# Performance work log

Measured on AMD Instinct MI355X. Metric: run time of the kernel, lower is better.

The kernel has to match this reference:

```python
import jax, jax.numpy as jnp
import numpy as np

EPS = 1e-5

def gamma_layer_norm(x, gamma):
    # LayerNorm over last dim with learnable gamma only (no bias)
    mu = jnp.mean(x, axis=-1, keepdims=True)
    var = jnp.var(x, axis=-1, keepdims=True)
    return (x - mu) * jax.lax.rsqrt(var + EPS) * gamma

def setup_inputs() -> dict:
    key = jax.random.key(0)
    k1, k2, k3, k4 = jax.random.split(key, 4)
    b, n, dim = 8, 4096, 512
    heads, head_size = 8, 64
    hidden = heads * head_size  # 512
    x = jax.random.normal(k1, (b, n, dim), dtype=jnp.float32)
    # nn.Linear(dim, hidden*3, bias=False): weight [3*hidden, dim]
    w_qkv = jax.random.normal(k2, (3 * hidden, dim), dtype=jnp.float32) * (dim ** -0.5)
    # nn.Linear(hidden, dim, bias=False): weight [dim, hidden]
    w_out = jax.random.normal(k3, (dim, hidden), dtype=jnp.float32) * (hidden ** -0.5)
    gamma = 1.0 + 0.02 * jax.random.normal(k4, (dim,), dtype=jnp.float32)
    return {"x": x, "w_qkv": w_qkv, "w_out": w_out, "gamma": gamma}

def reference(x, w_qkv, w_out, gamma):
    b, n, dim = x.shape
    heads, head_size = 8, 64
    scale = head_size ** -0.5
    # norm=False -> Identity; no time conditioning
    qkv = jnp.einsum('bnd,hd->bnh', x, w_qkv)  # [b, n, 3*hidden]
    q, k, v = jnp.split(qkv, 3, axis=-1)
    def to_heads(t):
        return t.reshape(b, n, heads, head_size).transpose(0, 2, 1, 3)  # b h n d
    q, k, v = to_heads(q), to_heads(k), to_heads(v)
    q = jax.nn.softmax(q, axis=-1) * scale   # softmax over feature dim
    k = jax.nn.softmax(k, axis=-2)           # softmax over sequence dim
    context = jnp.einsum('bhnd,bhne->bhde', k, v)      # [b, h, d, e]
    out = jnp.einsum('bhde,bhnd->bhne', context, q)    # [b, h, n, e]
    out = out.transpose(0, 2, 1, 3).reshape(b, n, heads * head_size)
    out = jnp.einsum('bnh,dh->bnd', out, w_out)
    out = gamma_layer_norm(out, gamma)  # dropout inactive (p=0 / eval)
    return out
```

## Files before the change

kernel.cpp:

```cpp
#include <hip/hip_runtime.h>
#include <hip/hip_bf16.h>
#include <stdint.h>
#include <stddef.h>

typedef __bf16 bf16_t;
typedef __bf16 bf16x8 __attribute__((ext_vector_type(8)));
typedef float floatx4 __attribute__((ext_vector_type(4)));

#define DIM 512
#define SEQ 4096
#define BATCH 8

static __device__ __forceinline__ floatx4 mfma_bf16(bf16x8 a, bf16x8 b, floatx4 c) {
  return __builtin_amdgcn_mfma_f32_16x16x32_bf16(a, b, c, 0, 0, 0);
}

typedef __attribute__((address_space(1))) const void* gas_ptr;
typedef __attribute__((address_space(3))) void* las_ptr;
static __device__ __forceinline__ void gll16(const void* g, void* l) {
  __builtin_amdgcn_global_load_lds((gas_ptr)g, (las_ptr)l, 16, 0, 0);
}

__global__ __launch_bounds__(256) void k_cvt(const float* __restrict__ w, bf16_t* __restrict__ wb) {
  int i = (blockIdx.x * 256 + threadIdx.x) * 8;
  float4 a = *(const float4*)&w[i];
  float4 b = *(const float4*)&w[i + 4];
  bf16x8 o;
  o[0] = (bf16_t)a.x; o[1] = (bf16_t)a.y; o[2] = (bf16_t)a.z; o[3] = (bf16_t)a.w;
  o[4] = (bf16_t)b.x; o[5] = (bf16_t)b.y; o[6] = (bf16_t)b.z; o[7] = (bf16_t)b.w;
  *(bf16x8*)&wb[i] = o;
}

__global__ __launch_bounds__(512, 2) void k_qkv(const bf16_t* __restrict__ Xb,
                                                const bf16_t* __restrict__ Wb,
                                                bf16_t* __restrict__ qs,
                                                bf16_t* __restrict__ ek,
                                                bf16_t* __restrict__ vb,
                                                float* __restrict__ S) {
  __shared__ __align__(16) bf16_t As[2][256 * 64];
  __shared__ __align__(16) bf16_t Bs[2][256 * 64];
  const int tid = threadIdx.x;
  const int lane = tid & 63;
  const int w = tid >> 6;
  const int wr = w >> 2, wc = w & 3;
  const int l15 = lane & 15, l4 = lane >> 4;
  const int m0 = blockIdx.x * 256;
  const int n0 = blockIdx.y * 256;

  int sr[4], su[4];
#pragma unroll
  for (int i = 0; i < 4; ++i) {
    int s = tid + i * 512;
    sr[i] = s >> 3;
    su[i] = ((s & 7) ^ (sr[i] & 7)) << 3;
  }

  floatx4 acc[8][4];
#pragma unroll
  for (int i = 0; i < 8; ++i)
#pragma unroll
    for (int j = 0; j < 4; ++j) acc[i][j] = (floatx4){0.f, 0.f, 0.f, 0.f};

#pragma unroll
  for (int i = 0; i < 4; ++i) {
    int s = tid + i * 512;
    gll16(Xb + (size_t)(m0 + sr[i]) * DIM + su[i], &As[0][s * 8]);
    gll16(Wb + (size_t)(n0 + sr[i]) * DIM + su[i], &Bs[0][s * 8]);
  }

  for (int t = 0; t < 8; ++t) {
    const int cur = t & 1;
    if (t < 7) {
      const int kt = (t + 1) * 64;
#pragma unroll
      for (int i = 0; i < 4; ++i) {
        int s = tid + i * 512;
        gll16(Xb + (size_t)(m0 + sr[i]) * DIM + kt + su[i], &As[cur ^ 1][s * 8]);
        gll16(Wb + (size_t)(n0 + sr[i]) * DIM + kt + su[i], &Bs[cur ^ 1][s * 8]);
      }
      asm volatile("s_waitcnt vmcnt(8)" ::: "memory");
    } else {
      asm volatile("s_waitcnt vmcnt(0)" ::: "memory");
    }
    __builtin_amdgcn_s_barrier();
    __builtin_amdgcn_sched_barrier(0);
    __builtin_amdgcn_s_setprio(1);
#pragma unroll
    for (int kk = 0; kk < 2; ++kk) {
      bf16x8 af[8], bfr[4];
#pragma unroll
      for (int f = 0; f < 8; ++f) {
        int ar = wr * 128 + f * 16 + l15;
        int ua = (kk * 4 + l4) ^ (ar & 7);
        af[f] = *(const bf16x8*)(&As[cur][ar * 64 + ua * 8]);
      }
#pragma unroll
      for (int f = 0; f < 4; ++f) {
        int br = wc * 64 + f * 16 + l15;
        int ub = (kk * 4 + l4) ^ (br & 7);
        bfr[f] = *(const bf16x8*)(&Bs[cur][br * 64 + ub * 8]);
      }
#pragma unroll
      for (int i = 0; i < 8; ++i)
#pragma unroll
        for (int j = 0; j < 4; ++j)
          acc[i][j] = mfma_bf16(af[i], bfr[j], acc[i][j]);
    }
    __builtin_amdgcn_s_setprio(0);
    __builtin_amdgcn_sched_barrier(0);
    __builtin_amdgcn_s_barrier();
  }

  const int colbase = n0 + wc * 64;
  if (n0 < 512) {
#pragma unroll
    for (int fm = 0; fm < 8; ++fm) {
#pragma unroll
      for (int r = 0; r < 4; ++r) {
        float v0 = acc[fm][0][r], v1 = acc[fm][1][r], v2 = acc[fm][2][r], v3 = acc[fm][3][r];
        float mx = fmaxf(fmaxf(v0, v1), fmaxf(v2, v3));
        mx = fmaxf(mx, __shfl_xor(mx, 1));
        mx = fmaxf(mx, __shfl_xor(mx, 2));
        mx = fmaxf(mx, __shfl_xor(mx, 4));
        mx = fmaxf(mx, __shfl_xor(mx, 8));
        float e0 = __expf(v0 - mx), e1 = __expf(v1 - mx), e2 = __expf(v2 - mx), e3 = __expf(v3 - mx);
        float s = e0 + e1 + e2 + e3;
        s += __shfl_xor(s, 1); s += __shfl_xor(s, 2); s += __shfl_xor(s, 4); s += __shfl_xor(s, 8);
        float inv = 0.125f / s;
        int m = m0 + wr * 128 + fm * 16 + l4 * 4 + r;
        bf16_t* rowp = qs + (size_t)m * DIM + colbase;
        rowp[l15]      = (bf16_t)(e0 * inv);
        rowp[16 + l15] = (bf16_t)(e1 * inv);
        rowp[32 + l15] = (bf16_t)(e2 * inv);
        rowp[48 + l15] = (bf16_t)(e3 * inv);
      }
    }
  } else if (n0 < 1024) {
    const int cb = colbase - 512;
    float c0 = 0.f, c1 = 0.f, c2 = 0.f, c3 = 0.f;
#pragma unroll
    for (int fm = 0; fm < 8; ++fm) {
#pragma unroll
      for (int r = 0; r < 4; ++r) {
        int m = m0 + wr * 128 + fm * 16 + l4 * 4 + r;
        bf16_t* rowp = ek + (size_t)m * DIM + cb;
        float e0 = __expf(acc[fm][0][r]);
        float e1 = __expf(acc[fm][1][r]);
        float e2 = __expf(acc[fm][2][r]);
        float e3 = __expf(acc[fm][3][r]);
        rowp[l15]      = (bf16_t)e0;
        rowp[16 + l15] = (bf16_t)e1;
        rowp[32 + l15] = (bf16_t)e2;
        rowp[48 + l15] = (bf16_t)e3;
        c0 += e0; c1 += e1; c2 += e2; c3 += e3;
      }
    }
    c0 += __shfl_xor(c0, 16); c0 += __shfl_xor(c0, 32);
    c1 += __shfl_xor(c1, 16); c1 += __shfl_xor(c1, 32);
    c2 += __shfl_xor(c2, 16); c2 += __shfl_xor(c2, 32);
    c3 += __shfl_xor(c3, 16); c3 += __shfl_xor(c3, 32);
    if (lane < 16) {
      int b = m0 >> 12;
      atomicAdd(&S[b * 512 + cb + lane],      c0);
      atomicAdd(&S[b * 512 + cb + 16 + lane], c1);
      atomicAdd(&S[b * 512 + cb + 32 + lane], c2);
      atomicAdd(&S[b * 512 + cb + 48 + lane], c3);
    }
  } else {
    const int cb = colbase - 1024;
#pragma unroll
    for (int fm = 0; fm < 8; ++fm) {
#pragma unroll
      for (int r = 0; r < 4; ++r) {
        int m = m0 + wr * 128 + fm * 16 + l4 * 4 + r;
        bf16_t* rowp = vb + (size_t)m * DIM + cb;
        rowp[l15]      = (bf16_t)acc[fm][0][r];
        rowp[16 + l15] = (bf16_t)acc[fm][1][r];
        rowp[32 + l15] = (bf16_t)acc[fm][2][r];
        rowp[48 + l15] = (bf16_t)acc[fm][3][r];
      }
    }
  }
}

#define TP 136
__global__ __launch_bounds__(256) void k_ctx(const bf16_t* __restrict__ ek,
                                             const bf16_t* __restrict__ vb,
                                             float* __restrict__ ctxpart) {
  __shared__ __align__(16) bf16_t ekT[64 * TP];
  __shared__ __align__(16) bf16_t vT[64 * TP];
  __shared__ float red[4096];
  const int tid = threadIdx.x;
  const int lane = tid & 63, wid = tid >> 6;
  const int l15 = lane & 15, l4 = lane >> 4;
  const int bh = blockIdx.x, chunk = blockIdx.y;
  const int b = bh >> 3, h = bh & 7;
  const int base = b * SEQ + chunk * 512;

  floatx4 acc[4][4];
#pragma unroll
  for (int i = 0; i < 4; ++i)
#pragma unroll
    for (int j = 0; j < 4; ++j) acc[i][j] = (floatx4){0.f, 0.f, 0.f, 0.f};

  for (int nt = 0; nt < 4; ++nt) {
    const int n0 = base + nt * 128;
    if (nt) __syncthreads();
#pragma unroll
    for (int i = 0; i < 4; ++i) {
      int q = tid + i * 256;
      int n = q >> 3;
      int u = q & 7;
      bf16x8 vk = *(const bf16x8*)&ek[(size_t)(n0 + n) * DIM + h * 64 + u * 8];
      bf16x8 vv = *(const bf16x8*)&vb[(size_t)(n0 + n) * DIM + h * 64 + u * 8];
      int ncol = n ^ (u << 3);
#pragma unroll
      for (int j = 0; j < 8; ++j) {
        int c = u * 8 + j;
        ekT[c * TP + ncol] = vk[j];
        vT [c * TP + ncol] = vv[j];
      }
    }
    __syncthreads();
    const int nb = wid * 32;
    bf16x8 af[4], bfr[4];
#pragma unroll
    for (int f = 0; f < 4; ++f) {
      int c = f * 16 + l15;
      int colstart = (nb + l4 * 8) ^ (((c >> 3) & 7) << 3);
      af[f]  = *(const bf16x8*)&ekT[c * TP + colstart];
      bfr[f] = *(const bf16x8*)&vT [c * TP + colstart];
    }
#pragma unroll
    for (int i = 0; i < 4; ++i)
#pragma unroll
      for (int j = 0; j < 4; ++j)
        acc[i][j] = mfma_bf16(af[i], bfr[j], acc[i][j]);
  }

  __syncthreads();
  for (int w = 0; w < 4; ++w) {
    if (wid == w) {
#pragma unroll
      for (int fm = 0; fm < 4; ++fm)
#pragma unroll
        for (int fn = 0; fn < 4; ++fn)
#pragma unroll
          for (int r = 0; r < 4; ++r) {
            int d = fm * 16 + l4 * 4 + r;
            int e = fn * 16 + l15;
            if (w == 0) red[d * 64 + e] = acc[fm][fn][r];
            else        red[d * 64 + e] += acc[fm][fn][r];
          }
    }
    __syncthreads();
  }
  float* dst = ctxpart + ((size_t)bh * 8 + chunk) * 4096;
#pragma unroll
  for (int i = 0; i < 4; ++i) {
    int q = tid + i * 256;
    *(float4*)&dst[q * 4] = *(const float4*)&red[q * 4];
  }
}

__global__ __launch_bounds__(256) void k_mt(const float* __restrict__ ctxpart,
                                            const float* __restrict__ S,
                                            const float* __restrict__ w_out,
                                            bf16_t* __restrict__ Mt) {
  __shared__ float cs[4096];
  const int tid = threadIdx.x;
  const int bh = blockIdx.x;
  const int b = bh >> 3, h = bh & 7;
#pragma unroll
  for (int i = 0; i < 16; ++i) {
    int idx = tid + i * 256;
    float s = 0.f;
#pragma unroll
    for (int p = 0; p < 8; ++p) s += ctxpart[((size_t)bh * 8 + p) * 4096 + idx];
    cs[idx] = s / S[b * 512 + h * 64 + (idx >> 6)];
  }
  __syncthreads();
  for (int half = 0; half < 2; ++half) {
    const int dcol = half * 256 + tid;
    float a[64];
#pragma unroll
    for (int d = 0; d < 64; ++d) a[d] = 0.f;
    for (int e = 0; e < 64; ++e) {
      float we = w_out[(size_t)dcol * 512 + h * 64 + e];
#pragma unroll
      for (int d = 0; d < 64; ++d) a[d] += cs[d * 64 + e] * we;
    }
    bf16_t* dst = Mt + ((size_t)b * 512 + dcol) * 512 + h * 64;
#pragma unroll
    for (int g = 0; g < 8; ++g) {
      bf16x8 o;
#pragma unroll
      for (int j = 0; j < 8; ++j) o[j] = (bf16_t)a[g * 8 + j];
      *(bf16x8*)&dst[g * 8] = o;
    }
  }
}

__global__ __launch_bounds__(512, 2) void k_out(const bf16_t* __restrict__ qs,
                                                const bf16_t* __restrict__ Mt,
                                                const float* __restrict__ gamma,
                                                float* __restrict__ out) {
  __shared__ __align__(16) bf16_t As[128 * 64];
  __shared__ __align__(16) bf16_t Bs[512 * 64];
  __shared__ float redS[128 * 4];
  __shared__ float redQ[128 * 4];
  const int tid = threadIdx.x;
  const int lane = tid & 63;
  const int w = tid >> 6;
  const int wr = w >> 2, wc = w & 3;
  const int l15 = lane & 15, l4 = lane >> 4;
  const int m0 = blockIdx.x * 128;
  const bf16_t* Bp = Mt + (size_t)(blockIdx.x >> 5) * 512 * 512;

  floatx4 acc[4][8];
#pragma unroll
  for (int i = 0; i < 4; ++i)
#pragma unroll
    for (int j = 0; j < 8; ++j) acc[i][j] = (floatx4){0.f, 0.f, 0.f, 0.f};

  for (int kt = 0; kt < 512; kt += 64) {
#pragma unroll
    for (int i = 0; i < 2; ++i) {
      int s = tid + i * 512;
      int r = s >> 3;
      int u = ((s & 7) ^ (r & 7)) << 3;
      gll16(qs + (size_t)(m0 + r) * 512 + kt + u, &As[s * 8]);
    }
#pragma unroll
    for (int i = 0; i < 8; ++i) {
      int s = tid + i * 512;
      int r = s >> 3;
      int u = ((s & 7) ^ (r & 7)) << 3;
      gll16(Bp + (size_t)r * 512 + kt + u, &Bs[s * 8]);
    }
    __syncthreads();
#pragma unroll
    for (int kk = 0; kk < 2; ++kk) {
      bf16x8 af[4], bfr[8];
#pragma unroll
      for (int f = 0; f < 4; ++f) {
        int ar = wr * 64 + f * 16 + l15;
        int ua = (kk * 4 + l4) ^ (ar & 7);
        af[f] = *(const bf16x8*)(&As[ar * 64 + ua * 8]);
      }
#pragma unroll
      for (int f = 0; f < 8; ++f) {
        int br = wc * 128 + f * 16 + l15;
        int ub = (kk * 4 + l4) ^ (br & 7);
        bfr[f] = *(const bf16x8*)(&Bs[br * 64 + ub * 8]);
      }
#pragma unroll
      for (int i = 0; i < 4; ++i)
#pragma unroll
        for (int j = 0; j < 8; ++j)
          acc[i][j] = mfma_bf16(af[i], bfr[j], acc[i][j]);
    }
    __syncthreads();
  }

#pragma unroll
  for (int fm = 0; fm < 4; ++fm) {
#pragma unroll
    for (int r = 0; r < 4; ++r) {
      float s = 0.f, q = 0.f;
#pragma unroll
      for (int fn = 0; fn < 8; ++fn) {
        float v = acc[fm][fn][r];
        s += v; q += v * v;
      }
      s += __shfl_xor(s, 1); q += __shfl_xor(q, 1);
      s += __shfl_xor(s, 2); q += __shfl_xor(q, 2);
      s += __shfl_xor(s, 4); q += __shfl_xor(q, 4);
      s += __shfl_xor(s, 8); q += __shfl_xor(q, 8);
      if (l15 == 0) {
        int rl = wr * 64 + fm * 16 + l4 * 4 + r;
        redS[rl * 4 + wc] = s;
        redQ[rl * 4 + wc] = q;
      }
    }
  }
  __syncthreads();
  float gm[8];
#pragma unroll
  for (int fn = 0; fn < 8; ++fn) gm[fn] = gamma[wc * 128 + fn * 16 + l15];
#pragma unroll
  for (int fm = 0; fm < 4; ++fm) {
#pragma unroll
    for (int r = 0; r < 4; ++r) {
      int rl = wr * 64 + fm * 16 + l4 * 4 + r;
      float4 sv = *(const float4*)&redS[rl * 4];
      float4 qv = *(const float4*)&redQ[rl * 4];
      float Sr = sv.x + sv.y + sv.z + sv.w;
      float Qr = qv.x + qv.y + qv.z + qv.w;
      float mean = Sr * (1.f / 512.f);
      float var = Qr * (1.f / 512.f) - mean * mean;
      float rstd = rsqrtf(var + 1e-5f);
      float* rowp = out + (size_t)(m0 + rl) * 512 + wc * 128 + l15;
#pragma unroll
      for (int fn = 0; fn < 8; ++fn)
        rowp[fn * 16] = (acc[fm][fn][r] - mean) * rstd * gm[fn];
    }
  }
}

extern "C" void kernel_launch(void* const* d_in, const int* in_sizes, int n_in,
                              void* d_out, int out_size, void* d_ws, size_t ws_size,
                              hipStream_t stream) {
  const float* x     = (const float*)d_in[0];
  const float* w_qkv = (const float*)d_in[1];
  const float* w_out = (const float*)d_in[2];
  const float* gamma = (const float*)d_in[3];
  float* out = (float*)d_out;
  char* ws = (char*)d_ws;

  bf16_t* qs      = (bf16_t*)(ws);
  bf16_t* ek      = (bf16_t*)(ws + 33554432);
  bf16_t* vb      = (bf16_t*)(ws + 67108864);
  bf16_t* wqkvb   = (bf16_t*)(ws + 100663296);
  float*  S       = (float*)(ws + 102236160);
  bf16_t* Xb      = (bf16_t*)(ws + 102252544);
  float*  ctxpart = (float*)(ws + 103301120);
  bf16_t* Mt      = (bf16_t*)(ws + 111689728);

  hipMemsetAsync(S, 0, BATCH * 512 * sizeof(float), stream);

  k_cvt<<<384, 256, 0, stream>>>(w_qkv, wqkvb);
  k_cvt<<<8192, 256, 0, stream>>>(x, Xb);

  dim3 g1(128, 6);
  k_qkv<<<g1, 512, 0, stream>>>(Xb, wqkvb, qs, ek, vb, S);

  dim3 g2(64, 8);
  k_ctx<<<g2, 256, 0, stream>>>(ek, vb, ctxpart);

  k_mt<<<64, 256, 0, stream>>>(ctxpart, S, w_out, Mt);

  k_out<<<256, 512, 0, stream>>>(qs, Mt, gamma, out);
}
```

Measured before the change: 196.8 us.

## Halve K-tile to 32 in QKV and output GEMMs, double-buffer output GEMM

The QKV GEMM's K tile drops from 64 to 32, halving its LDS footprint (64 KB to 32 KB per block), which could allow more resident blocks per CU. A new packed, swizzled layout stores two rows' 32-element K chunks per 64-wide LDS row. The output GEMM switches from a single-buffered loop with __syncthreads to a double-buffered async global_load_lds pipeline with waitcnt, raised priority and explicit barriers, so loads overlap compute. The cost is twice as many loop iterations and barriers per GEMM.

New measurement: 214.0 us. +8.7%, slower.

```diff
diff --git a/kernel.cpp b/kernel.cpp
--- a/kernel.cpp
+++ b/kernel.cpp
@@ -37,8 +37,8 @@
                                                 bf16_t* __restrict__ ek,
                                                 bf16_t* __restrict__ vb,
                                                 float* __restrict__ S) {
-  __shared__ __align__(16) bf16_t As[2][256 * 64];
-  __shared__ __align__(16) bf16_t Bs[2][256 * 64];
+  __shared__ __align__(16) bf16_t As[2][128 * 64];
+  __shared__ __align__(16) bf16_t Bs[2][128 * 64];
   const int tid = threadIdx.x;
   const int lane = tid & 63;
   const int w = tid >> 6;
@@ -47,12 +47,14 @@
   const int m0 = blockIdx.x * 256;
   const int n0 = blockIdx.y * 256;
 
-  int sr[4], su[4];
-#pragma unroll
-  for (int i = 0; i < 4; ++i) {
+  int srow[2], skc[2];
+#pragma unroll
+  for (int i = 0; i < 2; ++i) {
     int s = tid + i * 512;
-    sr[i] = s >> 3;
-    su[i] = ((s & 7) ^ (sr[i] & 7)) << 3;
+    int R = s >> 3, p = s & 7;
+    int g = p ^ (R & 7);
+    srow[i] = 2 * R + (g >> 2);
+    skc[i] = (g & 3) << 3;
   }
 
   floatx4 acc[8][4];
@@ -62,43 +64,44 @@
     for (int j = 0; j < 4; ++j) acc[i][j] = (floatx4){0.f, 0.f, 0.f, 0.f};
 
 #pragma unroll
-  for (int i = 0; i < 4; ++i) {
+  for (int i = 0; i < 2; ++i) {
     int s = tid + i * 512;
-    gll16(Xb + (size_t)(m0 + sr[i]) * DIM + su[i], &As[0][s * 8]);
-    gll16(Wb + (size_t)(n0 + sr[i]) * DIM + su[i], &Bs[0][s * 8]);
-  }
-
-  for (int t = 0; t < 8; ++t) {
+    gll16(Xb + (size_t)(m0 + srow[i]) * DIM + skc[i], &As[0][s * 8]);
+    gll16(Wb + (size_t)(n0 + srow[i]) * DIM + skc[i], &Bs[0][s * 8]);
+  }
+
+  for (int t = 0; t < 16; ++t) {
     const int cur = t & 1;
-    if (t < 7) {
-      const int kt = (t + 1) * 64;
-#pragma unroll
-      for (int i = 0; i < 4; ++i) {
+    if (t < 15) {
+      const int kt = (t + 1) * 32;
+#pragma unroll
+      for (int i = 0; i < 2; ++i) {
         int s = tid + i * 512;
-        gll16(Xb + (size_t)(m0 + sr[i]) * DIM + kt + su[i], &As[cur ^ 1][s * 8]);
-        gll16(Wb + (size_t)(n0 + sr[i]) * DIM + kt + su[i], &Bs[cur ^ 1][s * 8]);
-      }
-      asm volatile("s_waitcnt vmcnt(8)" ::: "memory");
+        gll16(Xb + (size_t)(m0 + srow[i]) * DIM + kt + skc[i], &As[cur ^ 1][s * 8]);
+        gll16(Wb + (size_t)(n0 + srow[i]) * DIM + kt + skc[i], &Bs[cur ^ 1][s * 8]);
+      }
+      asm volatile("s_waitcnt vmcnt(4)" ::: "memory");
     } else {
       asm volatile("s_waitcnt vmcnt(0)" ::: "memory");
     }
     __builtin_amdgcn_s_barrier();
     __builtin_amdgcn_sched_barrier(0);
     __builtin_amdgcn_s_setprio(1);
-#pragma unroll
-    for (int kk = 0; kk < 2; ++kk) {
+    {
       bf16x8 af[8], bfr[4];
 #pragma unroll
       for (int f = 0; f < 8; ++f) {
         int ar = wr * 128 + f * 16 + l15;
-        int ua = (kk * 4 + l4) ^ (ar & 7);
-        af[f] = *(const bf16x8*)(&As[cur][ar * 64 + ua * 8]);
+        int R = ar >> 1;
+        int p = (((ar & 1) << 2) + l4) ^ (R & 7);
+        af[f] = *(const bf16x8*)(&As[cur][R * 64 + p * 8]);
       }
 #pragma unroll
       for (int f = 0; f < 4; ++f) {
         int br = wc * 64 + f * 16 + l15;
-        int ub = (kk * 4 + l4) ^ (br & 7);
-        bfr[f] = *(const bf16x8*)(&Bs[cur][br * 64 + ub * 8]);
+        int R = br >> 1;
+        int p = (((br & 1) << 2) + l4) ^ (R & 7);
+        bfr[f] = *(const bf16x8*)(&Bs[cur][R * 64 + p * 8]);
       }
 #pragma unroll
       for (int i = 0; i < 8; ++i)
@@ -305,8 +308,8 @@
                                                 const bf16_t* __restrict__ Mt,
                                                 const float* __restrict__ gamma,
                                                 float* __restrict__ out) {
-  __shared__ __align__(16) bf16_t As[128 * 64];
-  __shared__ __align__(16) bf16_t Bs[512 * 64];
+  __shared__ __align__(16) bf16_t As[2][64 * 64];
+  __shared__ __align__(16) bf16_t Bs[2][256 * 64];
   __shared__ float redS[128 * 4];
   __shared__ float redQ[128 * 4];
   const int tid = threadIdx.x;
@@ -317,42 +320,64 @@
   const int m0 = blockIdx.x * 128;
   const bf16_t* Bp = Mt + (size_t)(blockIdx.x >> 5) * 512 * 512;
 
+  int aRow, aKc;
+  {
+    int R = tid >> 3, p = tid & 7;
+    int g = p ^ (R & 7);
+    aRow = 2 * R + (g >> 2);
+    aKc = (g & 3) << 3;
+  }
+  int bRow[4], bKc[4];
+#pragma unroll
+  for (int i = 0; i < 4; ++i) {
+    int s = tid + i * 512;
+    int R = s >> 3, p = s & 7;
+    int g = p ^ (R & 7);
+    bRow[i] = 2 * R + (g >> 2);
+    bKc[i] = (g & 3) << 3;
+  }
+
   floatx4 acc[4][8];
 #pragma unroll
   for (int i = 0; i < 4; ++i)
 #pragma unroll
     for (int j = 0; j < 8; ++j) acc[i][j] = (floatx4){0.f, 0.f, 0.f, 0.f};
 
-  for (int kt = 0; kt < 512; kt += 64) {
-#pragma unroll
-    for (int i = 0; i < 2; ++i) {
-      int s = tid + i * 512;
-      int r = s >> 3;
-      int u = ((s & 7) ^ (r & 7)) << 3;
-      gll16(qs + (size_t)(m0 + r) * 512 + kt + u, &As[s * 8]);
-    }
-#pragma unroll
-    for (int i = 0; i < 8; ++i) {
-      int s = tid + i * 512;
-      int r = s >> 3;
-      int u = ((s & 7) ^ (r & 7)) << 3;
-      gll16(Bp + (size_t)r * 512 + kt + u, &Bs[s * 8]);
-    }
-    __syncthreads();
-#pragma unroll
-    for (int kk = 0; kk < 2; ++kk) {
+  gll16(qs + (size_t)(m0 + aRow) * 512 + aKc, &As[0][tid * 8]);
+#pragma unroll
+  for (int i = 0; i < 4; ++i)
+    gll16(Bp + (size_t)bRow[i] * 512 + bKc[i], &Bs[0][(tid + i * 512) * 8]);
+
+  for (int t = 0; t < 16; ++t) {
+    const int cur = t & 1;
+    if (t < 15) {
+      const int kt = (t + 1) * 32;
+      gll16(qs + (size_t)(m0 + aRow) * 512 + kt + aKc, &As[cur ^ 1][tid * 8]);
+#pragma unroll
+      for (int i = 0; i < 4; ++i)
+        gll16(Bp + (size_t)bRow[i] * 512 + kt + bKc[i], &Bs[cur ^ 1][(tid + i * 512) * 8]);
+      asm volatile("s_waitcnt vmcnt(5)" ::: "memory");
+    } else {
+      asm volatile("s_waitcnt vmcnt(0)" ::: "memory");
+    }
+    __builtin_amdgcn_s_barrier();
+    __builtin_amdgcn_sched_barrier(0);
+    __builtin_amdgcn_s_setprio(1);
+    {
       bf16x8 af[4], bfr[8];
 #pragma unroll
       for (int f = 0; f < 4; ++f) {
         int ar = wr * 64 + f * 16 + l15;
-        int ua = (kk * 4 + l4) ^ (ar & 7);
-        af[f] = *(const bf16x8*)(&As[ar * 64 + ua * 8]);
+        int R = ar >> 1;
+        int p = (((ar & 1) << 2) + l4) ^ (R & 7);
+        af[f] = *(const bf16x8*)(&As[cur][R * 64 + p * 8]);
       }
 #pragma unroll
       for (int f = 0; f < 8; ++f) {
         int br = wc * 128 + f * 16 + l15;
-        int ub = (kk * 4 + l4) ^ (br & 7);
-        bfr[f] = *(const bf16x8*)(&Bs[br * 64 + ub * 8]);
+        int R = br >> 1;
+        int p = (((br & 1) << 2) + l4) ^ (R & 7);
+        bfr[f] = *(const bf16x8*)(&Bs[cur][R * 64 + p * 8]);
       }
 #pragma unroll
       for (int i = 0; i < 4; ++i)
@@ -360,7 +385,9 @@
         for (int j = 0; j < 8; ++j)
           acc[i][j] = mfma_bf16(af[i], bfr[j], acc[i][j]);
     }
-    __syncthreads();
+    __builtin_amdgcn_s_setprio(0);
+    __builtin_amdgcn_sched_barrier(0);
+    __builtin_amdgcn_s_barrier();
   }
 
 #pragma unroll
```

## Pipeline k_out loads with double-buffered A and register-staged B; merge convert kernels

Applied to the files above, without the earlier changes.

Merges the two fp32-to-bf16 conversion launches into one kernel that picks its source by block index, removing one launch. In the output GEMM, the A tile becomes double-buffered through direct global-to-LDS loads. The B tile is prefetched into registers during compute and written to LDS after a barrier, so global latency overlaps the MFMA work. This adds register pressure and extra barriers, and could reduce occupancy in k_out.

Measured after the change: 196.7 us. No clear change (-0.1%).

```diff
diff --git a/kernel.cpp b/kernel.cpp
--- a/kernel.cpp
+++ b/kernel.cpp
@@ -21,14 +21,20 @@
   __builtin_amdgcn_global_load_lds((gas_ptr)g, (las_ptr)l, 16, 0, 0);
 }
 
-__global__ __launch_bounds__(256) void k_cvt(const float* __restrict__ w, bf16_t* __restrict__ wb) {
-  int i = (blockIdx.x * 256 + threadIdx.x) * 8;
-  float4 a = *(const float4*)&w[i];
-  float4 b = *(const float4*)&w[i + 4];
+__global__ __launch_bounds__(256) void k_cvt2(const float* __restrict__ w, bf16_t* __restrict__ wb,
+                                              const float* __restrict__ x, bf16_t* __restrict__ xb) {
+  const float* src;
+  bf16_t* dst;
+  int blk = blockIdx.x;
+  if (blk < 384) { src = w; dst = wb; }
+  else           { src = x; dst = xb; blk -= 384; }
+  int i = (blk * 256 + threadIdx.x) * 8;
+  float4 a = *(const float4*)&src[i];
+  float4 b = *(const float4*)&src[i + 4];
   bf16x8 o;
   o[0] = (bf16_t)a.x; o[1] = (bf16_t)a.y; o[2] = (bf16_t)a.z; o[3] = (bf16_t)a.w;
   o[4] = (bf16_t)b.x; o[5] = (bf16_t)b.y; o[6] = (bf16_t)b.z; o[7] = (bf16_t)b.w;
-  *(bf16x8*)&wb[i] = o;
+  *(bf16x8*)&dst[i] = o;
 }
 
 __global__ __launch_bounds__(512, 2) void k_qkv(const bf16_t* __restrict__ Xb,
@@ -305,7 +311,7 @@
                                                 const bf16_t* __restrict__ Mt,
                                                 const float* __restrict__ gamma,
                                                 float* __restrict__ out) {
-  __shared__ __align__(16) bf16_t As[128 * 64];
+  __shared__ __align__(16) bf16_t As[2][128 * 64];
   __shared__ __align__(16) bf16_t Bs[512 * 64];
   __shared__ float redS[128 * 4];
   __shared__ float redQ[128 * 4];
@@ -317,28 +323,53 @@
   const int m0 = blockIdx.x * 128;
   const bf16_t* Bp = Mt + (size_t)(blockIdx.x >> 5) * 512 * 512;
 
+  int aR[2], aU[2];
+#pragma unroll
+  for (int i = 0; i < 2; ++i) {
+    int s = tid + i * 512;
+    aR[i] = s >> 3;
+    aU[i] = ((s & 7) ^ (aR[i] & 7)) << 3;
+  }
+  int bR[8], bU[8];
+#pragma unroll
+  for (int i = 0; i < 8; ++i) {
+    int s = tid + i * 512;
+    bR[i] = s >> 3;
+    bU[i] = ((s & 7) ^ (bR[i] & 7)) << 3;
+  }
+
   floatx4 acc[4][8];
 #pragma unroll
   for (int i = 0; i < 4; ++i)
 #pragma unroll
     for (int j = 0; j < 8; ++j) acc[i][j] = (floatx4){0.f, 0.f, 0.f, 0.f};
 
-  for (int kt = 0; kt < 512; kt += 64) {
-#pragma unroll
-    for (int i = 0; i < 2; ++i) {
-      int s = tid + i * 512;
-      int r = s >> 3;
-      int u = ((s & 7) ^ (r & 7)) << 3;
-      gll16(qs + (size_t)(m0 + r) * 512 + kt + u, &As[s * 8]);
-    }
-#pragma unroll
-    for (int i = 0; i < 8; ++i) {
-      int s = tid + i * 512;
-      int r = s >> 3;
-      int u = ((s & 7) ^ (r & 7)) << 3;
-      gll16(Bp + (size_t)r * 512 + kt + u, &Bs[s * 8]);
-    }
-    __syncthreads();
+  bf16x8 breg[8];
+#pragma unroll
+  for (int i = 0; i < 2; ++i)
+    gll16(qs + (size_t)(m0 + aR[i]) * 512 + aU[i], &As[0][(tid + i * 512) * 8]);
+#pragma unroll
+  for (int i = 0; i < 8; ++i)
+    breg[i] = *(const bf16x8*)(Bp + (size_t)bR[i] * 512 + bU[i]);
+  asm volatile("s_waitcnt vmcnt(0)" ::: "memory");
+#pragma unroll
+  for (int i = 0; i < 8; ++i)
+    *(bf16x8*)(&Bs[(tid + i * 512) * 8]) = breg[i];
+  asm volatile("s_waitcnt lgkmcnt(0)" ::: "memory");
+  __builtin_amdgcn_s_barrier();
+
+  for (int t = 0; t < 8; ++t) {
+    const int cur = t & 1;
+    if (t < 7) {
+      const int kt = (t + 1) * 64;
+#pragma unroll
+      for (int i = 0; i < 2; ++i)
+        gll16(qs + (size_t)(m0 + aR[i]) * 512 + kt + aU[i], &As[cur ^ 1][(tid + i * 512) * 8]);
+#pragma unroll
+      for (int i = 0; i < 8; ++i)
+        breg[i] = *(const bf16x8*)(Bp + (size_t)bR[i] * 512 + kt + bU[i]);
+    }
+    __builtin_amdgcn_s_setprio(1);
 #pragma unroll
     for (int kk = 0; kk < 2; ++kk) {
       bf16x8 af[4], bfr[8];
@@ -346,7 +377,7 @@
       for (int f = 0; f < 4; ++f) {
         int ar = wr * 64 + f * 16 + l15;
         int ua = (kk * 4 + l4) ^ (ar & 7);
-        af[f] = *(const bf16x8*)(&As[ar * 64 + ua * 8]);
+        af[f] = *(const bf16x8*)(&As[cur][ar * 64 + ua * 8]);
       }
 #pragma unroll
       for (int f = 0; f < 8; ++f) {
@@ -360,7 +391,17 @@
         for (int j = 0; j < 8; ++j)
           acc[i][j] = mfma_bf16(af[i], bfr[j], acc[i][j]);
     }
-    __syncthreads();
+    __builtin_amdgcn_s_setprio(0);
+    __builtin_amdgcn_sched_barrier(0);
+    __builtin_amdgcn_s_barrier();
+    if (t < 7) {
+      asm volatile("s_waitcnt vmcnt(0)" ::: "memory");
+#pragma unroll
+      for (int i = 0; i < 8; ++i)
+        *(bf16x8*)(&Bs[(tid + i * 512) * 8]) = breg[i];
+      asm volatile("s_waitcnt lgkmcnt(0)" ::: "memory");
+      __builtin_amdgcn_s_barrier();
+    }
   }
 
 #pragma unroll
@@ -429,8 +470,7 @@
 
   hipMemsetAsync(S, 0, BATCH * 512 * sizeof(float), stream);
 
-  k_cvt<<<384, 256, 0, stream>>>(w_qkv, wqkvb);
-  k_cvt<<<8192, 256, 0, stream>>>(x, Xb);
+  k_cvt2<<<8576, 256, 0, stream>>>(w_qkv, wqkvb, x, Xb);
 
   dim3 g1(128, 6);
   k_qkv<<<g1, 512, 0, stream>>>(Xb, wqkvb, qs, ek, vb, S);
```
